# Performance work log

Hardware: AMD Instinct MI355X
Metric: run time of the kernel (lower is better)

The kernel has to match this reference:

```python
import jax, jax.numpy as jnp
import numpy as np

# Module constants derived from default grid_config
D = 59          # depth bins: (60-1)/1
C_OUT = 64
X, Y, Z = 128, 128, 7
STRIDE = 16
GRID_LB = np.array([-51.2, -51.2, -2.5], dtype=np.float32)
GRID_IV = np.array([0.8, 0.8, 1.0], dtype=np.float32)
D0, DSTEP = 1.0, 1.0

B, N, C_IN, H, W = 4, 6, 256, 16, 44


def _voxel_coords():
    xs, ys, zs = np.meshgrid(np.arange(X), np.arange(Y), np.arange(Z), indexing='ij')
    coords = np.stack([xs, ys, zs], axis=-1).reshape(-1, 3).astype(np.float32)
    coords = coords * GRID_IV + GRID_LB  # [V, 3] ego-frame voxel centers
    return coords


def _camera_rig(rng):
    """Realistic 6-camera rig: yawed cameras looking outward, z_cam = forward."""
    c2e = np.zeros((B, N, 4, 4), dtype=np.float32)
    K = np.zeros((B, N, 3, 3), dtype=np.float32)
    for b in range(B):
        for n in range(N):
            a = 2.0 * np.pi * n / N + 0.02 * rng.standard_normal()
            f = np.array([np.cos(a), np.sin(a), 0.0])           # camera forward (z_cam)
            x_cam = np.array([-np.sin(a), np.cos(a), 0.0])      # camera right
            y_cam = np.array([0.0, 0.0, -1.0])                   # camera down
            R = np.stack([x_cam, y_cam, f], axis=1)              # columns = cam axes in ego
            t = 1.0 * f + np.array([0.0, 0.0, 1.5])
            c2e[b, n, :3, :3] = R
            c2e[b, n, :3, 3] = t
            c2e[b, n, 3, 3] = 1.0
            fl = 400.0 + 5.0 * rng.standard_normal()
            K[b, n] = np.array([[fl, 0.0, 352.0], [0.0, fl, 128.0], [0.0, 0.0, 1.0]])
    return c2e, K


def setup_inputs() -> dict:
    key = jax.random.key(0)
    k1, k2, k3 = jax.random.split(key, 3)
    img_feats = jax.random.normal(k1, (B, N, C_IN, H, W), dtype=jnp.float32)
    c2e, K = _camera_rig(np.random.default_rng(0))
    # depth_net: 1x1 conv in_channels -> D + C_OUT
    w_depth = jax.random.normal(k2, (D + C_OUT, C_IN), dtype=jnp.float32) * (1.0 / np.sqrt(C_IN))
    b_depth = jax.random.normal(k3, (D + C_OUT,), dtype=jnp.float32) * 0.01
    return {
        'img_feats': img_feats,
        'cam2ego': jnp.asarray(c2e),
        'cam_intrinsics': jnp.asarray(K),
        'w_depth': w_depth,
        'b_depth': b_depth,
    }


def reference(img_feats, cam2ego, cam_intrinsics, w_depth, b_depth):
    Bc, Nc, C, Hc, Wc = img_feats.shape
    # 1x1 conv == per-pixel linear
    x = jnp.einsum('bnchw,oc->bnhwo', img_feats, w_depth) + b_depth  # [B,N,H,W,D+C_OUT]
    depth = jax.nn.softmax(x[..., :D], axis=-1)                      # [B,N,H,W,D]
    feat = x[..., D:]                                                # [B,N,H,W,C_OUT]

    vox = jnp.asarray(_voxel_coords())                               # [V,3]
    V = vox.shape[0]
    vox_h = jnp.concatenate([vox, jnp.ones((V, 1), vox.dtype)], axis=1)  # [V,4]

    e2c = jnp.linalg.inv(cam2ego)                                    # [B,N,4,4]
    cam = jnp.einsum('bnij,vj->bnvi', e2c, vox_h)[..., :3]           # [B,N,V,3]
    z = cam[..., 2]
    z_safe = jnp.maximum(z, 0.1)
    norm = cam[..., :2] / z_safe[..., None]
    homo = jnp.concatenate([norm, jnp.ones_like(z[..., None])], axis=-1)  # [B,N,V,3]
    img = jnp.einsum('bnij,bnvj->bnvi', cam_intrinsics, homo)[..., :2]
    fc = img / STRIDE                                                # feature-plane coords

    depth_bin = ((z - D0) / DSTEP).astype(jnp.int32)                 # trunc toward 0, matches .long()
    valid = (
        (fc[..., 0] >= 0) & (fc[..., 0] < Wc)
        & (fc[..., 1] >= 0) & (fc[..., 1] < Hc)
        & (z > 0.5)
        & (depth_bin >= 0) & (depth_bin < D)
    )

    u = jnp.clip(fc[..., 0].astype(jnp.int32), 0, Wc - 1)            # [B,N,V]
    v = jnp.clip(fc[..., 1].astype(jnp.int32), 0, Hc - 1)
    d = jnp.clip(depth_bin, 0, D - 1)
    hw = v * Wc + u

    feat_flat = feat.reshape(Bc, Nc, Hc * Wc, C_OUT)
    sampled_feat = jnp.take_along_axis(feat_flat, hw[..., None], axis=2)   # [B,N,V,C_OUT]
    depth_flat = depth.reshape(Bc, Nc, Hc * Wc * D)
    sampled_depth = jnp.take_along_axis(depth_flat, hw * D + d, axis=2)    # [B,N,V]

    wgt = sampled_depth * valid.astype(sampled_depth.dtype)
    # scatter_add at flat_idx == voxel index (identity) -> masked sum over cameras
    bev = jnp.einsum('bnv,bnvc->bvc', wgt, sampled_feat)             # [B,V,C_OUT]
    bev = bev.reshape(Bc, X, Y, Z, C_OUT).sum(axis=3)                # collapse Z
    bev = bev.transpose(0, 3, 2, 1)                                  # [B,C_OUT,Y,X]
    return bev, depth
```

## Files before the change

### kernel.cpp

```cpp
#include <hip/hip_runtime.h>
#include <math.h>

#define D_BINS 59
#define CO     64
#define CI     256
#define NB     4
#define NC     6
#define H_IMG  16
#define W_IMG  44
#define HW     704
#define NPIX   (NB*NC*HW)
#define XD     128
#define YD     128
#define ZD     7
#define NOUT   123
#define PXB    66

typedef float v2f __attribute__((ext_vector_type(2)));

__device__ void inv_rigid(const float* __restrict__ M, float* __restrict__ o) {
    double a = M[0], b = M[1], c = M[2], t0 = M[3];
    double d = M[4], e = M[5], f = M[6], t1 = M[7];
    double g = M[8], h = M[9], ii = M[10], t2 = M[11];
    double A00 = e*ii - f*h, A01 = c*h - b*ii, A02 = b*f - c*e;
    double A10 = f*g - d*ii, A11 = a*ii - c*g, A12 = c*d - a*f;
    double A20 = d*h - e*g,  A21 = b*g - a*h,  A22 = a*e - b*d;
    double det = a*A00 + b*A10 + c*A20;
    double inv = 1.0 / det;
    double r00 = A00*inv, r01 = A01*inv, r02 = A02*inv;
    double r10 = A10*inv, r11 = A11*inv, r12 = A12*inv;
    double r20 = A20*inv, r21 = A21*inv, r22 = A22*inv;
    o[0] = (float)r00; o[1] = (float)r01; o[2]  = (float)r02;
    o[3] = (float)(-(r00*t0 + r01*t1 + r02*t2));
    o[4] = (float)r10; o[5] = (float)r11; o[6]  = (float)r12;
    o[7] = (float)(-(r10*t0 + r11*t1 + r12*t2));
    o[8] = (float)r20; o[9] = (float)r21; o[10] = (float)r22;
    o[11] = (float)(-(r20*t0 + r21*t1 + r22*t2));
}

__global__ __launch_bounds__(256) void k_pre(
    const float* __restrict__ wd, const float* __restrict__ c2e,
    float* __restrict__ wt2, float* __restrict__ e2c) {
    const int o = blockIdx.x;
    const int k = threadIdx.x;
    float v = (o < NOUT) ? wd[(size_t)o * CI + k] : 0.f;
    wt2[(size_t)(k >> 1) * 256 + o * 2 + (k & 1)] = v;
    if (blockIdx.x == 0 && k < NB * NC)
        inv_rigid(c2e + k * 16, e2c + k * 12);
}

__global__ __launch_bounds__(640) void k_head(
    const float* __restrict__ img, const float* __restrict__ wt2,
    const float* __restrict__ bd, float* __restrict__ depth_out,
    float* __restrict__ feat_ws) {
    __shared__ float smem[PXB * 132 + PXB];
    float* S = smem + PXB * 132;

    const int tid = threadIdx.x;
    const int wv  = tid >> 6;
    const int ln  = tid & 63;
    const int p0  = blockIdx.x * PXB;
    const bool is_main = (wv < 8);
    const int o0  = __builtin_amdgcn_readfirstlane((is_main ? wv : 0) << 4);
    const int epx = 64 + (wv - 8);

    v2f acc[16];
#pragma unroll
    for (int j = 0; j < 16; ++j) acc[j] = (v2f)(0.f);
    v2f acc2a = (v2f)(0.f), acc2b = (v2f)(0.f);

    for (int kc = 0; kc < 4; ++kc) {
#pragma unroll
        for (int it = 0; it < 7; ++it) {
            int idx = tid + it * 640;
            if (idx < 64 * PXB) {
                int kl = idx / PXB, px = idx - kl * PXB;
                int p = p0 + px;
                int bn = p / HW, hw = p - bn * HW;
                smem[(kl >> 1) * 132 + px * 2 + (kl & 1)] =
                    img[((size_t)bn * CI + kc * 64 + kl) * HW + hw];
            }
        }
        __syncthreads();
        if (is_main) {
#pragma unroll 4
            for (int k2 = 0; k2 < 32; ++k2) {
                v2f a = *(const v2f*)(smem + k2 * 132 + ln * 2);
                const v2f* w =
                    (const v2f*)(wt2 + (size_t)(kc * 32 + k2) * 256) + o0;
#pragma unroll
                for (int j = 0; j < 16; ++j)
                    acc[j] = __builtin_elementwise_fma(a, w[j], acc[j]);
            }
        } else {
#pragma unroll 4
            for (int k2 = 0; k2 < 32; ++k2) {
                v2f a = *(const v2f*)(smem + k2 * 132 + epx * 2);
                const float* w = wt2 + (size_t)(kc * 32 + k2) * 256;
                v2f w0 = {w[ln * 2], w[ln * 2 + 1]};
                v2f w1 = {w[(ln + 64) * 2], w[(ln + 64) * 2 + 1]};
                acc2a = __builtin_elementwise_fma(a, w0, acc2a);
                acc2b = __builtin_elementwise_fma(a, w1, acc2b);
            }
        }
        __syncthreads();
    }

    float* X = smem;
    if (is_main) {
#pragma unroll
        for (int j = 0; j < 16; ++j) {
            int o = o0 + j;
            if (o < NOUT) {
                int col = (o < D_BINS) ? o : o + 5;
                X[ln * 132 + col] = (acc[j].x + acc[j].y) + bd[o];
            }
        }
    } else {
        int o = ln;
        X[epx * 132 + ((o < D_BINS) ? o : o + 5)] = (acc2a.x + acc2a.y) + bd[o];
        o = ln + 64;
        if (o < NOUT)
            X[epx * 132 + ((o < D_BINS) ? o : o + 5)] = (acc2b.x + acc2b.y) + bd[o];
    }
    __syncthreads();

#pragma unroll
    for (int it = 0; it < 2; ++it) {
        int g = tid + it * 640;
        if (g < PXB * 16) {
            int p = g >> 4, m = g & 15;
            float4 v = *(const float4*)(X + p * 132 + 64 + m * 4);
            *(float4*)(feat_ws + (size_t)(p0 + p) * CO + m * 4) = v;
        }
    }

    if (tid < PXB) {
        float* row = X + tid * 132;
        float m = row[0];
        for (int o = 1; o < D_BINS; ++o) m = fmaxf(m, row[o]);
        float s = 0.f;
        for (int o = 0; o < D_BINS; ++o) {
            float e = __expf(row[o] - m);
            row[o] = e;
            s += e;
        }
        S[tid] = 1.f / s;
    }
    __syncthreads();

    for (int g = tid; g < PXB * D_BINS; g += 640) {
        int p = g / D_BINS;
        int o = g - p * D_BINS;
        depth_out[(size_t)p0 * D_BINS + g] = X[p * 132 + o] * S[p];
    }
}

__global__ __launch_bounds__(256) void k_splat(
    const float* __restrict__ e2c, const float* __restrict__ Kmat,
    const float* __restrict__ depth_g, const float* __restrict__ feat_ws,
    float* __restrict__ bev) {
    __shared__ int   hw_s[ZD][64];
    __shared__ float wgt_s[ZD][64];

    const int tx = threadIdx.x;
    const int cq = threadIdx.y;
    const int x = blockIdx.x * 64 + tx;
    const int y = blockIdx.y;
    const int b = blockIdx.z;
    const float wx = (float)x * 0.8f + (-51.2f);
    const float wy = (float)y * 0.8f + (-51.2f);

    float acc[16];
#pragma unroll
    for (int m = 0; m < 16; ++m) acc[m] = 0.f;

    for (int n = 0; n < NC; ++n) {
        const int bn = b * NC + n;
        const float* E = e2c + bn * 12;
        const float* Km = Kmat + bn * 9;
        const float k00 = Km[0], k01 = Km[1], k02 = Km[2];
        const float k10 = Km[3], k11 = Km[4], k12 = Km[5];
        const float e02 = E[2], e12 = E[6], e22 = E[10];
        const float bx0 = E[0] * wx + E[1] * wy + E[3];
        const float bx1 = E[4] * wx + E[5] * wy + E[7];
        const float bx2 = E[8] * wx + E[9] * wy + E[11];

#pragma unroll
        for (int zz = 0; zz < 2; ++zz) {
            const int z = cq + zz * 4;
            if (z < ZD) {
                const float wz = -2.5f + (float)z;
                const float cx = bx0 + e02 * wz;
                const float cy = bx1 + e12 * wz;
                const float cz = bx2 + e22 * wz;
                const float zs = fmaxf(cz, 0.1f);
                const float rz = 1.0f / zs;
                const float xn = cx * rz;
                const float yn = cy * rz;
                const float fu = (k00 * xn + k01 * yn + k02) * 0.0625f;
                const float fv = (k10 * xn + k11 * yn + k12) * 0.0625f;
                const int bin = (int)(cz - 1.0f);
                const bool valid = (fu >= 0.f) & (fu < (float)W_IMG) &
                                   (fv >= 0.f) & (fv < (float)H_IMG) &
                                   (cz > 0.5f) & (bin >= 0) & (bin < D_BINS);
                int hw = -1;
                float wgt = 0.f;
                if (valid) {
                    int u = (int)fu;
                    int v = (int)fv;
                    hw = v * W_IMG + u;
                    wgt = depth_g[((size_t)bn * HW + hw) * D_BINS + bin];
                }
                hw_s[z][tx] = hw;
                wgt_s[z][tx] = wgt;
            }
        }
        __syncthreads();

#pragma unroll
        for (int z = 0; z < ZD; ++z) {
            const int hw = hw_s[z][tx];
            if (hw >= 0) {
                const float wgt = wgt_s[z][tx];
                const float4* fp =
                    (const float4*)(feat_ws + ((size_t)bn * HW + hw) * CO + cq * 16);
                float4 f0 = fp[0], f1 = fp[1], f2 = fp[2], f3 = fp[3];
                acc[0]  = fmaf(wgt, f0.x, acc[0]);
                acc[1]  = fmaf(wgt, f0.y, acc[1]);
                acc[2]  = fmaf(wgt, f0.z, acc[2]);
                acc[3]  = fmaf(wgt, f0.w, acc[3]);
                acc[4]  = fmaf(wgt, f1.x, acc[4]);
                acc[5]  = fmaf(wgt, f1.y, acc[5]);
                acc[6]  = fmaf(wgt, f1.z, acc[6]);
                acc[7]  = fmaf(wgt, f1.w, acc[7]);
                acc[8]  = fmaf(wgt, f2.x, acc[8]);
                acc[9]  = fmaf(wgt, f2.y, acc[9]);
                acc[10] = fmaf(wgt, f2.z, acc[10]);
                acc[11] = fmaf(wgt, f2.w, acc[11]);
                acc[12] = fmaf(wgt, f3.x, acc[12]);
                acc[13] = fmaf(wgt, f3.y, acc[13]);
                acc[14] = fmaf(wgt, f3.z, acc[14]);
                acc[15] = fmaf(wgt, f3.w, acc[15]);
            }
        }
        __syncthreads();
    }
    float* ob = bev + (((size_t)b * CO + cq * 16) * YD + y) * XD + x;
#pragma unroll
    for (int m = 0; m < 16; ++m) ob[(size_t)m * YD * XD] = acc[m];
}

extern "C" void kernel_launch(void* const* d_in, const int* in_sizes, int n_in,
                              void* d_out, int out_size, void* d_ws, size_t ws_size,
                              hipStream_t stream) {
    const float* img  = (const float*)d_in[0];
    const float* c2e  = (const float*)d_in[1];
    const float* Kmat = (const float*)d_in[2];
    const float* wd   = (const float*)d_in[3];
    const float* bd   = (const float*)d_in[4];
    float* bev = (float*)d_out;
    float* depth_out = bev + (size_t)NB * CO * YD * XD;
    float* feat_ws = (float*)d_ws;
    float* wt2 = feat_ws + (size_t)NPIX * CO;
    float* e2c = wt2 + 128 * 256;

    k_pre<<<128, 256, 0, stream>>>(wd, c2e, wt2, e2c);
    k_head<<<256, 640, 0, stream>>>(img, wt2, bd, depth_out, feat_ws);
    k_splat<<<dim3(2, YD, NB), dim3(64, 4, 1), 0, stream>>>(e2c, Kmat, depth_out,
                                                            feat_ws, bev);
}
```

Baseline: 124.2 us.

## Drop weight-transpose pre-kernel; read weights directly and invert extrinsics in splat

Removes the k_pre launch that transposed the depth-net weights and inverted the camera extrinsics. k_head now reads the original row-major weights directly, with the loop order changed so each output row is streamed contiguously over k while 32 activation pairs stay in registers. k_splat inverts the six cam2ego matrices per block into shared memory. This saves one kernel launch and a global round trip, at the cost of higher register pressure in k_head, wavefront-uniform weight loads replacing coalesced broadcast ones, and redundant per-block matrix inversions in double precision.

```diff
diff --git a/kernel.cpp b/kernel.cpp
--- a/kernel.cpp
+++ b/kernel.cpp
@@ -38,19 +38,8 @@
     o[11] = (float)(-(r20*t0 + r21*t1 + r22*t2));
 }
 
-__global__ __launch_bounds__(256) void k_pre(
-    const float* __restrict__ wd, const float* __restrict__ c2e,
-    float* __restrict__ wt2, float* __restrict__ e2c) {
-    const int o = blockIdx.x;
-    const int k = threadIdx.x;
-    float v = (o < NOUT) ? wd[(size_t)o * CI + k] : 0.f;
-    wt2[(size_t)(k >> 1) * 256 + o * 2 + (k & 1)] = v;
-    if (blockIdx.x == 0 && k < NB * NC)
-        inv_rigid(c2e + k * 16, e2c + k * 12);
-}
-
 __global__ __launch_bounds__(640) void k_head(
-    const float* __restrict__ img, const float* __restrict__ wt2,
+    const float* __restrict__ img, const float* __restrict__ wd,
     const float* __restrict__ bd, float* __restrict__ depth_out,
     float* __restrict__ feat_ws) {
     __shared__ float smem[PXB * 132 + PXB];
@@ -83,24 +72,30 @@
         }
         __syncthreads();
         if (is_main) {
-#pragma unroll 4
-            for (int k2 = 0; k2 < 32; ++k2) {
-                v2f a = *(const v2f*)(smem + k2 * 132 + ln * 2);
-                const v2f* w =
-                    (const v2f*)(wt2 + (size_t)(kc * 32 + k2) * 256) + o0;
-#pragma unroll
-                for (int j = 0; j < 16; ++j)
-                    acc[j] = __builtin_elementwise_fma(a, w[j], acc[j]);
+            v2f a[32];
+#pragma unroll
+            for (int k2 = 0; k2 < 32; ++k2)
+                a[k2] = *(const v2f*)(smem + k2 * 132 + ln * 2);
+#pragma unroll
+            for (int j = 0; j < 16; ++j) {
+                int o = o0 + j;
+                if (o < NOUT) {
+                    const v2f* w = (const v2f*)(wd + (size_t)o * CI + kc * 64);
+#pragma unroll
+                    for (int k2 = 0; k2 < 32; ++k2)
+                        acc[j] = __builtin_elementwise_fma(a[k2], w[k2], acc[j]);
+                }
             }
         } else {
 #pragma unroll 4
             for (int k2 = 0; k2 < 32; ++k2) {
-                v2f a = *(const v2f*)(smem + k2 * 132 + epx * 2);
-                const float* w = wt2 + (size_t)(kc * 32 + k2) * 256;
-                v2f w0 = {w[ln * 2], w[ln * 2 + 1]};
-                v2f w1 = {w[(ln + 64) * 2], w[(ln + 64) * 2 + 1]};
-                acc2a = __builtin_elementwise_fma(a, w0, acc2a);
-                acc2b = __builtin_elementwise_fma(a, w1, acc2b);
+                v2f av = *(const v2f*)(smem + k2 * 132 + epx * 2);
+                v2f w0 = *(const v2f*)(wd + (size_t)ln * CI + kc * 64 + k2 * 2);
+                acc2a = __builtin_elementwise_fma(av, w0, acc2a);
+                if (ln + 64 < NOUT) {
+                    v2f w1 = *(const v2f*)(wd + (size_t)(ln + 64) * CI + kc * 64 + k2 * 2);
+                    acc2b = __builtin_elementwise_fma(av, w1, acc2b);
+                }
             }
         }
         __syncthreads();
@@ -157,17 +152,23 @@
 }
 
 __global__ __launch_bounds__(256) void k_splat(
-    const float* __restrict__ e2c, const float* __restrict__ Kmat,
+    const float* __restrict__ c2e, const float* __restrict__ Kmat,
     const float* __restrict__ depth_g, const float* __restrict__ feat_ws,
     float* __restrict__ bev) {
     __shared__ int   hw_s[ZD][64];
     __shared__ float wgt_s[ZD][64];
+    __shared__ float E_s[NC][12];
 
     const int tx = threadIdx.x;
     const int cq = threadIdx.y;
     const int x = blockIdx.x * 64 + tx;
     const int y = blockIdx.y;
     const int b = blockIdx.z;
+
+    if (cq == 0 && tx < NC)
+        inv_rigid(c2e + (size_t)(b * NC + tx) * 16, &E_s[tx][0]);
+    __syncthreads();
+
     const float wx = (float)x * 0.8f + (-51.2f);
     const float wy = (float)y * 0.8f + (-51.2f);
 
@@ -177,7 +178,7 @@
 
     for (int n = 0; n < NC; ++n) {
         const int bn = b * NC + n;
-        const float* E = e2c + bn * 12;
+        const float* E = &E_s[n][0];
         const float* Km = Kmat + bn * 9;
         const float k00 = Km[0], k01 = Km[1], k02 = Km[2];
         const float k10 = Km[3], k11 = Km[4], k12 = Km[5];
@@ -262,11 +263,8 @@
     float* bev = (float*)d_out;
     float* depth_out = bev + (size_t)NB * CO * YD * XD;
     float* feat_ws = (float*)d_ws;
-    float* wt2 = feat_ws + (size_t)NPIX * CO;
-    float* e2c = wt2 + 128 * 256;
-
-    k_pre<<<128, 256, 0, stream>>>(wd, c2e, wt2, e2c);
-    k_head<<<256, 640, 0, stream>>>(img, wt2, bd, depth_out, feat_ws);
-    k_splat<<<dim3(2, YD, NB), dim3(64, 4, 1), 0, stream>>>(e2c, Kmat, depth_out,
+
+    k_head<<<256, 640, 0, stream>>>(img, wd, bd, depth_out, feat_ws);
+    k_splat<<<dim3(2, YD, NB), dim3(64, 4, 1), 0, stream>>>(c2e, Kmat, depth_out,
                                                             feat_ws, bev);
 }
```

Result: slower. 140.7 us (+13.2%).

## Retile depth head to 64-pixel blocks and fold camera inverse into splat

Applied to the files above, without the earlier changes.

The depth/feature head now handles 64 pixels per block with 1024 threads (16 waves, 8 outputs each). This replaces the old 66-pixel layout, which split work unevenly between main and extra waves. Because 704 is a multiple of 64, a block never spans two cameras, so the image load is a simple contiguous strided read without per-element div/mod. The rigid-transform inverse moves out of the pre-kernel and into each splat block's shared memory, which removes a global dependency but repeats a small amount of work per block. The tighter launch bounds may limit registers available to the GEMM loop.

```diff
diff --git a/kernel.cpp b/kernel.cpp
--- a/kernel.cpp
+++ b/kernel.cpp
@@ -14,7 +14,6 @@
 #define YD     128
 #define ZD     7
 #define NOUT   123
-#define PXB    66
 
 typedef float v2f __attribute__((ext_vector_type(2)));
 
@@ -39,103 +38,73 @@
 }
 
 __global__ __launch_bounds__(256) void k_pre(
-    const float* __restrict__ wd, const float* __restrict__ c2e,
-    float* __restrict__ wt2, float* __restrict__ e2c) {
+    const float* __restrict__ wd, float* __restrict__ wt2) {
     const int o = blockIdx.x;
     const int k = threadIdx.x;
     float v = (o < NOUT) ? wd[(size_t)o * CI + k] : 0.f;
     wt2[(size_t)(k >> 1) * 256 + o * 2 + (k & 1)] = v;
-    if (blockIdx.x == 0 && k < NB * NC)
-        inv_rigid(c2e + k * 16, e2c + k * 12);
-}
-
-__global__ __launch_bounds__(640) void k_head(
+}
+
+__global__ __launch_bounds__(1024, 8) void k_head(
     const float* __restrict__ img, const float* __restrict__ wt2,
     const float* __restrict__ bd, float* __restrict__ depth_out,
     float* __restrict__ feat_ws) {
-    __shared__ float smem[PXB * 132 + PXB];
-    float* S = smem + PXB * 132;
+    __shared__ float smem[64 * 132 + 64];
+    float* S = smem + 64 * 132;
 
     const int tid = threadIdx.x;
     const int wv  = tid >> 6;
     const int ln  = tid & 63;
-    const int p0  = blockIdx.x * PXB;
-    const bool is_main = (wv < 8);
-    const int o0  = __builtin_amdgcn_readfirstlane((is_main ? wv : 0) << 4);
-    const int epx = 64 + (wv - 8);
-
-    v2f acc[16];
-#pragma unroll
-    for (int j = 0; j < 16; ++j) acc[j] = (v2f)(0.f);
-    v2f acc2a = (v2f)(0.f), acc2b = (v2f)(0.f);
+    const int p0  = blockIdx.x * 64;
+    const int bn  = p0 / HW;
+    const int hw0 = p0 - bn * HW;
+    const int o0  = __builtin_amdgcn_readfirstlane(wv << 3);
+
+    const float* imgb = img + (size_t)bn * CI * HW + hw0;
+
+    v2f acc[8];
+#pragma unroll
+    for (int j = 0; j < 8; ++j) acc[j] = (v2f)(0.f);
 
     for (int kc = 0; kc < 4; ++kc) {
 #pragma unroll
-        for (int it = 0; it < 7; ++it) {
-            int idx = tid + it * 640;
-            if (idx < 64 * PXB) {
-                int kl = idx / PXB, px = idx - kl * PXB;
-                int p = p0 + px;
-                int bn = p / HW, hw = p - bn * HW;
-                smem[(kl >> 1) * 132 + px * 2 + (kl & 1)] =
-                    img[((size_t)bn * CI + kc * 64 + kl) * HW + hw];
-            }
-        }
-        __syncthreads();
-        if (is_main) {
+        for (int it = 0; it < 4; ++it) {
+            int i = tid + it * 1024;
+            int kl = i >> 6, px = i & 63;
+            smem[(kl >> 1) * 130 + px * 2 + (kl & 1)] =
+                imgb[(size_t)(kc * 64 + kl) * HW + px];
+        }
+        __syncthreads();
 #pragma unroll 4
-            for (int k2 = 0; k2 < 32; ++k2) {
-                v2f a = *(const v2f*)(smem + k2 * 132 + ln * 2);
-                const v2f* w =
-                    (const v2f*)(wt2 + (size_t)(kc * 32 + k2) * 256) + o0;
-#pragma unroll
-                for (int j = 0; j < 16; ++j)
-                    acc[j] = __builtin_elementwise_fma(a, w[j], acc[j]);
-            }
-        } else {
-#pragma unroll 4
-            for (int k2 = 0; k2 < 32; ++k2) {
-                v2f a = *(const v2f*)(smem + k2 * 132 + epx * 2);
-                const float* w = wt2 + (size_t)(kc * 32 + k2) * 256;
-                v2f w0 = {w[ln * 2], w[ln * 2 + 1]};
-                v2f w1 = {w[(ln + 64) * 2], w[(ln + 64) * 2 + 1]};
-                acc2a = __builtin_elementwise_fma(a, w0, acc2a);
-                acc2b = __builtin_elementwise_fma(a, w1, acc2b);
-            }
+        for (int k2 = 0; k2 < 32; ++k2) {
+            v2f a = *(const v2f*)(smem + k2 * 130 + ln * 2);
+            const v2f* w =
+                (const v2f*)(wt2 + (size_t)(kc * 32 + k2) * 256) + o0;
+#pragma unroll
+            for (int j = 0; j < 8; ++j)
+                acc[j] = __builtin_elementwise_fma(a, w[j], acc[j]);
         }
         __syncthreads();
     }
 
     float* X = smem;
-    if (is_main) {
-#pragma unroll
-        for (int j = 0; j < 16; ++j) {
-            int o = o0 + j;
-            if (o < NOUT) {
-                int col = (o < D_BINS) ? o : o + 5;
-                X[ln * 132 + col] = (acc[j].x + acc[j].y) + bd[o];
-            }
-        }
-    } else {
-        int o = ln;
-        X[epx * 132 + ((o < D_BINS) ? o : o + 5)] = (acc2a.x + acc2a.y) + bd[o];
-        o = ln + 64;
-        if (o < NOUT)
-            X[epx * 132 + ((o < D_BINS) ? o : o + 5)] = (acc2b.x + acc2b.y) + bd[o];
+#pragma unroll
+    for (int j = 0; j < 8; ++j) {
+        int o = o0 + j;
+        if (o < NOUT) {
+            int col = (o < D_BINS) ? o : o + 5;
+            X[ln * 132 + col] = (acc[j].x + acc[j].y) + bd[o];
+        }
     }
     __syncthreads();
 
-#pragma unroll
-    for (int it = 0; it < 2; ++it) {
-        int g = tid + it * 640;
-        if (g < PXB * 16) {
-            int p = g >> 4, m = g & 15;
-            float4 v = *(const float4*)(X + p * 132 + 64 + m * 4);
-            *(float4*)(feat_ws + (size_t)(p0 + p) * CO + m * 4) = v;
-        }
-    }
-
-    if (tid < PXB) {
+    {
+        int p = tid >> 4, m = tid & 15;
+        float4 v = *(const float4*)(X + p * 132 + 64 + m * 4);
+        *(float4*)(feat_ws + (size_t)(p0 + p) * CO + m * 4) = v;
+    }
+
+    if (tid < 64) {
         float* row = X + tid * 132;
         float m = row[0];
         for (int o = 1; o < D_BINS; ++o) m = fmaxf(m, row[o]);
@@ -149,7 +118,7 @@
     }
     __syncthreads();
 
-    for (int g = tid; g < PXB * D_BINS; g += 640) {
+    for (int g = tid; g < 64 * D_BINS; g += 1024) {
         int p = g / D_BINS;
         int o = g - p * D_BINS;
         depth_out[(size_t)p0 * D_BINS + g] = X[p * 132 + o] * S[p];
@@ -157,17 +126,23 @@
 }
 
 __global__ __launch_bounds__(256) void k_splat(
-    const float* __restrict__ e2c, const float* __restrict__ Kmat,
+    const float* __restrict__ c2e, const float* __restrict__ Kmat,
     const float* __restrict__ depth_g, const float* __restrict__ feat_ws,
     float* __restrict__ bev) {
     __shared__ int   hw_s[ZD][64];
     __shared__ float wgt_s[ZD][64];
+    __shared__ float E_s[NC][12];
 
     const int tx = threadIdx.x;
     const int cq = threadIdx.y;
     const int x = blockIdx.x * 64 + tx;
     const int y = blockIdx.y;
     const int b = blockIdx.z;
+
+    if (cq == 0 && tx < NC)
+        inv_rigid(c2e + (size_t)(b * NC + tx) * 16, &E_s[tx][0]);
+    __syncthreads();
+
     const float wx = (float)x * 0.8f + (-51.2f);
     const float wy = (float)y * 0.8f + (-51.2f);
 
@@ -177,7 +152,7 @@
 
     for (int n = 0; n < NC; ++n) {
         const int bn = b * NC + n;
-        const float* E = e2c + bn * 12;
+        const float* E = &E_s[n][0];
         const float* Km = Kmat + bn * 9;
         const float k00 = Km[0], k01 = Km[1], k02 = Km[2];
         const float k10 = Km[3], k11 = Km[4], k12 = Km[5];
@@ -263,10 +238,9 @@
     float* depth_out = bev + (size_t)NB * CO * YD * XD;
     float* feat_ws = (float*)d_ws;
     float* wt2 = feat_ws + (size_t)NPIX * CO;
-    float* e2c = wt2 + 128 * 256;
-
-    k_pre<<<128, 256, 0, stream>>>(wd, c2e, wt2, e2c);
-    k_head<<<256, 640, 0, stream>>>(img, wt2, bd, depth_out, feat_ws);
-    k_splat<<<dim3(2, YD, NB), dim3(64, 4, 1), 0, stream>>>(e2c, Kmat, depth_out,
+
+    k_pre<<<128, 256, 0, stream>>>(wd, wt2);
+    k_head<<<NPIX / 64, 1024, 0, stream>>>(img, wt2, bd, depth_out, feat_ws);
+    k_splat<<<dim3(2, YD, NB), dim3(64, 4, 1), 0, stream>>>(c2e, Kmat, depth_out,
                                                             feat_ws, bev);
 }
```

New measurement: 132.3 us. 6.5% more time.
